# Kernel tuning notes

Hardware: AMD Instinct MI355X
Metric: run time of the kernel (lower is better)

Reference implementation:

```python
import jax, jax.numpy as jnp
import numpy as np


def quantize_ternary(w):
    # BitNet b1.58: scale by mean |w|, round, clamp to {-1,0,1}
    gamma = jnp.maximum(jnp.mean(jnp.abs(w)), 1e-8)
    return jnp.clip(jnp.round(w / gamma), -1.0, 1.0)


def setup_inputs() -> dict:
    key = jax.random.key(0)
    k1, k2, k3 = jax.random.split(key, 3)
    in_features, out_features = 4096, 4096
    x = jax.random.normal(k1, (4, 2048, in_features), dtype=jnp.float32)
    # kaiming_uniform-like init
    bound_w = 1.0 / np.sqrt(in_features)
    weight = jax.random.uniform(k2, (out_features, in_features), dtype=jnp.float32,
                                minval=-bound_w * np.sqrt(3.0), maxval=bound_w * np.sqrt(3.0))
    bias = jax.random.uniform(k3, (out_features,), dtype=jnp.float32,
                              minval=-bound_w, maxval=bound_w)
    return {"x": x, "weight": weight, "bias": bias}


def reference(x, weight, bias):
    qw = quantize_ternary(weight)  # [out, in], values in {-1,0,1}
    # F.linear: x @ qw.T + bias
    return jnp.einsum('bsi,oi->bso', x, qw) + bias
```

## Files before the change

### kernel.cpp

```cpp
#include <hip/hip_runtime.h>
#include <stdint.h>

#define M_DIM 8192
#define N_DIM 4096
#define K_DIM 4096
#define BM 256
#define BN 128
#define BKS 64
#define NSLAB (K_DIM / BKS)
#define A_SLOT (BM * BKS)
#define B_SLOT (BN * BKS)

typedef int i32x4 __attribute__((ext_vector_type(4)));

__device__ __forceinline__ void async_copy16(const void* g, void* l) {
    __builtin_amdgcn_global_load_lds(
        (const __attribute__((address_space(1))) void*)g,
        (__attribute__((address_space(3))) void*)l, 16, 0, 0);
}

__global__ __launch_bounds__(256) void prep_kernel(
    const float4* __restrict__ w,
    const float4* __restrict__ x,
    double* __restrict__ partials,
    char4* __restrict__ xq,
    float* __restrict__ xscale)
{
    const int lane = threadIdx.x & 63;
    const int wave = threadIdx.x >> 6;

    if (blockIdx.x < 1024) {
        int base = blockIdx.x * 4096 + threadIdx.x;
        float s = 0.f;
        #pragma unroll
        for (int i = 0; i < 16; i++) {
            float4 v = w[base + i * 256];
            s += fabsf(v.x) + fabsf(v.y) + fabsf(v.z) + fabsf(v.w);
        }
        double d = (double)s;
        #pragma unroll
        for (int off = 32; off > 0; off >>= 1) d += __shfl_down(d, off, 64);
        __shared__ double wsum[4];
        if (lane == 0) wsum[wave] = d;
        __syncthreads();
        if (threadIdx.x == 0)
            partials[blockIdx.x] = (wsum[0] + wsum[1]) + (wsum[2] + wsum[3]);
    } else {
        const int row = blockIdx.x - 1024;
        const float4* xr = x + (size_t)row * (K_DIM / 4);
        float4 v[4];
        float m = 0.f;
        #pragma unroll
        for (int i = 0; i < 4; i++) {
            v[i] = xr[threadIdx.x + i * 256];
            m = fmaxf(m, fmaxf(fmaxf(fabsf(v[i].x), fabsf(v[i].y)),
                               fmaxf(fabsf(v[i].z), fabsf(v[i].w))));
        }
        #pragma unroll
        for (int off = 32; off > 0; off >>= 1) m = fmaxf(m, __shfl_down(m, off, 64));
        __shared__ float wmax[4];
        if (lane == 0) wmax[wave] = m;
        __syncthreads();
        const float mx = fmaxf(fmaxf(wmax[0], wmax[1]), fmaxf(wmax[2], wmax[3]));
        const float scale = fmaxf(mx * (1.f / 127.f), 1e-30f);
        const float inv = 1.f / scale;
        if (threadIdx.x == 0) xscale[row] = scale;
        char4* oq = xq + (size_t)row * (K_DIM / 4);
        #pragma unroll
        for (int i = 0; i < 4; i++) {
            char4 o;
            o.x = (signed char)fminf(fmaxf(rintf(v[i].x * inv), -127.f), 127.f);
            o.y = (signed char)fminf(fmaxf(rintf(v[i].y * inv), -127.f), 127.f);
            o.z = (signed char)fminf(fmaxf(rintf(v[i].z * inv), -127.f), 127.f);
            o.w = (signed char)fminf(fmaxf(rintf(v[i].w * inv), -127.f), 127.f);
            oq[threadIdx.x + i * 256] = o;
        }
    }
}

__global__ __launch_bounds__(256) void wquant_kernel(
    const double* __restrict__ partials,
    const float4* __restrict__ w,
    char4* __restrict__ qw)
{
    const int lane = threadIdx.x & 63;
    const int wave = threadIdx.x >> 6;
    double d = partials[threadIdx.x] + partials[threadIdx.x + 256] +
               partials[threadIdx.x + 512] + partials[threadIdx.x + 768];
    #pragma unroll
    for (int off = 32; off > 0; off >>= 1) d += __shfl_down(d, off, 64);
    __shared__ double wsum[4];
    if (lane == 0) wsum[wave] = d;
    __shared__ float gsh;
    __syncthreads();
    if (threadIdx.x == 0) {
        double total = (wsum[0] + wsum[1]) + (wsum[2] + wsum[3]);
        gsh = fmaxf((float)(total * (1.0 / 16777216.0)), 1e-8f);
    }
    __syncthreads();
    const float gamma = gsh;

    int base = blockIdx.x * 4096 + threadIdx.x;
    #pragma unroll
    for (int j = 0; j < 16; j++) {
        float4 v = w[base + j * 256];
        char4 o;
        o.x = (signed char)fminf(fmaxf(rintf(v.x / gamma), -1.f), 1.f);
        o.y = (signed char)fminf(fmaxf(rintf(v.y / gamma), -1.f), 1.f);
        o.z = (signed char)fminf(fmaxf(rintf(v.z / gamma), -1.f), 1.f);
        o.w = (signed char)fminf(fmaxf(rintf(v.w / gamma), -1.f), 1.f);
        qw[base + j * 256] = o;
    }
}

__global__ __launch_bounds__(256, 2) void gemm_kernel(
    const char* __restrict__ xq,
    const char* __restrict__ qw,
    const float* __restrict__ xscale,
    const float* __restrict__ bias,
    float* __restrict__ out)
{
    __shared__ __align__(16) char As[3][A_SLOT];
    __shared__ __align__(16) char Bs[3][B_SLOT];

    const int tid  = threadIdx.x;
    const int wave = tid >> 6;
    const int lane = tid & 63;
    const int wm   = (wave >> 1) * 128;
    const int wn   = (wave & 1) * 64;
    const int lm   = lane & 15;
    const int q4   = lane >> 4;

    const int bm = blockIdx.y * BM;
    const int bn = blockIdx.x * BN;

    const int rsub = lane >> 2;
    const int csw  = (lane & 3) ^ ((lane >> 3) & 3);
    const char* gA[4];
    int ldsOffA[4];
    #pragma unroll
    for (int j = 0; j < 4; j++) {
        const int r = wave * 64 + j * 16 + rsub;
        gA[j] = xq + (size_t)(bm + r) * K_DIM + csw * 16;
        ldsOffA[j] = (wave * 64 + j * 16) * BKS;
    }
    const char* gB[2];
    int ldsOffB[2];
    #pragma unroll
    for (int j = 0; j < 2; j++) {
        const int r = wave * 32 + j * 16 + rsub;
        gB[j] = qw + (size_t)(bn + r) * K_DIM + csw * 16;
        ldsOffB[j] = (wave * 32 + j * 16) * BKS;
    }

    i32x4 acc[8][4];
    #pragma unroll
    for (int i = 0; i < 8; i++)
        #pragma unroll
        for (int j = 0; j < 4; j++) acc[i][j] = (i32x4){0, 0, 0, 0};

    const int pc = (q4 ^ ((lm >> 1) & 3)) * 16;

    auto stage_slab = [&](int ts, int slot) {
        #pragma unroll
        for (int j = 0; j < 4; j++)
            async_copy16(gA[j] + (size_t)ts * BKS, &As[slot][ldsOffA[j]]);
        #pragma unroll
        for (int j = 0; j < 2; j++)
            async_copy16(gB[j] + (size_t)ts * BKS, &Bs[slot][ldsOffB[j]]);
    };

    auto compute_slab = [&](const char* Ab, const char* Bb) {
        i32x4 b[4], a[8];
        #pragma unroll
        for (int ni = 0; ni < 4; ni++)
            b[ni] = *(const i32x4*)(Bb + (wn + ni * 16 + lm) * BKS + pc);
        #pragma unroll
        for (int mi = 0; mi < 8; mi++)
            a[mi] = *(const i32x4*)(Ab + (wm + mi * 16 + lm) * BKS + pc);
        __builtin_amdgcn_s_setprio(1);
        #pragma unroll
        for (int mi = 0; mi < 8; mi++)
            #pragma unroll
            for (int ni = 0; ni < 4; ni++)
                acc[mi][ni] = __builtin_amdgcn_mfma_i32_16x16x64_i8(
                    a[mi], b[ni], acc[mi][ni], 0, 0, 0);
        __builtin_amdgcn_s_setprio(0);
    };

    stage_slab(0, 0);
    stage_slab(1, 1);
    asm volatile("s_waitcnt vmcnt(6)" ::: "memory");
    __builtin_amdgcn_s_barrier();

    for (int tb = 0; tb < 60; tb += 3) {
        #pragma unroll
        for (int u = 0; u < 3; u++) {
            stage_slab(tb + u + 2, (u + 2) % 3);
            compute_slab(As[u], Bs[u]);
            asm volatile("s_waitcnt vmcnt(6)" ::: "memory");
            __builtin_amdgcn_s_barrier();
        }
    }

    stage_slab(62, 2);
    compute_slab(As[0], Bs[0]);
    asm volatile("s_waitcnt vmcnt(6)" ::: "memory");
    __builtin_amdgcn_s_barrier();

    stage_slab(63, 0);
    compute_slab(As[1], Bs[1]);
    asm volatile("s_waitcnt vmcnt(6)" ::: "memory");
    __builtin_amdgcn_s_barrier();

    compute_slab(As[2], Bs[2]);
    asm volatile("s_waitcnt vmcnt(0)" ::: "memory");
    __builtin_amdgcn_s_barrier();

    compute_slab(As[0], Bs[0]);

    float bl[4];
    #pragma unroll
    for (int ni = 0; ni < 4; ni++) bl[ni] = bias[bn + wn + ni * 16 + lm];

    #pragma unroll
    for (int mi = 0; mi < 8; mi++) {
        #pragma unroll
        for (int r = 0; r < 4; r++) {
            const int grow = bm + wm + mi * 16 + q4 * 4 + r;
            const float sc = xscale[grow];
            float* orow = out + (size_t)grow * N_DIM + bn + wn;
            #pragma unroll
            for (int ni = 0; ni < 4; ni++)
                orow[ni * 16 + lm] = sc * (float)acc[mi][ni][r] + bl[ni];
        }
    }
}

extern "C" void kernel_launch(void* const* d_in, const int* in_sizes, int n_in,
                              void* d_out, int out_size, void* d_ws, size_t ws_size,
                              hipStream_t stream) {
    const float* x    = (const float*)d_in[0];
    const float* w    = (const float*)d_in[1];
    const float* bias = (const float*)d_in[2];
    float* out = (float*)d_out;

    char* ws = (char*)d_ws;
    char*   xq       = ws;
    char*   qw       = ws + (size_t)M_DIM * K_DIM;
    float*  xscale   = (float*)(qw + (size_t)N_DIM * K_DIM);
    double* partials = (double*)(xscale + M_DIM);
    float*  gamma_p  = (float*)(partials + 1024);
    (void)gamma_p;

    prep_kernel<<<1024 + M_DIM, 256, 0, stream>>>(
        (const float4*)w, (const float4*)x, partials, (char4*)xq, xscale);
    wquant_kernel<<<1024, 256, 0, stream>>>(partials, (const float4*)w, (char4*)qw);

    dim3 grid(N_DIM / BN, M_DIM / BM);
    gemm_kernel<<<grid, 256, 0, stream>>>(xq, qw, xscale, bias, out);
}
```

Baseline: 410.5 us.

## Use 256x256 tiles with 32x32x32 int8 MFMA and register double-buffered fragments

The GEMM tile grows from 256x128 to 256x256 and switches from 16x16x64 to 32x32x32 int8 MFMA, which raises arithmetic intensity per LDS byte and halves the number of blocks. The LDS ring goes from three to four slots and stages three slabs ahead. Fragments for the next slab are read into a second register buffer while MFMAs run on the current one, with sched_barriers enforcing the order. Occupancy drops to one block per CU and register pressure rises, and the swizzle and epilogue row mapping change to match the new layout.

```diff
diff --git a/kernel.cpp b/kernel.cpp
--- a/kernel.cpp
+++ b/kernel.cpp
@@ -5,13 +5,13 @@
 #define N_DIM 4096
 #define K_DIM 4096
 #define BM 256
-#define BN 128
+#define BN 256
 #define BKS 64
 #define NSLAB (K_DIM / BKS)
-#define A_SLOT (BM * BKS)
-#define B_SLOT (BN * BKS)
-
-typedef int i32x4 __attribute__((ext_vector_type(4)));
+#define SLOT_BYTES (256 * BKS)
+
+typedef int i32x4  __attribute__((ext_vector_type(4)));
+typedef int i32x16 __attribute__((ext_vector_type(16)));
 
 __device__ __forceinline__ void async_copy16(const void* g, void* l) {
     __builtin_amdgcn_global_load_lds(
@@ -113,126 +113,150 @@
     }
 }
 
-__global__ __launch_bounds__(256, 2) void gemm_kernel(
+__global__ __launch_bounds__(256, 1) void gemm_kernel(
     const char* __restrict__ xq,
     const char* __restrict__ qw,
     const float* __restrict__ xscale,
     const float* __restrict__ bias,
     float* __restrict__ out)
 {
-    __shared__ __align__(16) char As[3][A_SLOT];
-    __shared__ __align__(16) char Bs[3][B_SLOT];
+    __shared__ __align__(16) char As[4][SLOT_BYTES];
+    __shared__ __align__(16) char Bs[4][SLOT_BYTES];
 
     const int tid  = threadIdx.x;
     const int wave = tid >> 6;
     const int lane = tid & 63;
     const int wm   = (wave >> 1) * 128;
-    const int wn   = (wave & 1) * 64;
-    const int lm   = lane & 15;
-    const int q4   = lane >> 4;
+    const int wn   = (wave & 1) * 128;
+    const int l31  = lane & 31;
+    const int lhi  = lane >> 5;
 
     const int bm = blockIdx.y * BM;
     const int bn = blockIdx.x * BN;
 
     const int rsub = lane >> 2;
-    const int csw  = (lane & 3) ^ ((lane >> 3) & 3);
+    const int csw  = (lane & 3) ^ ((lane >> 2) & 3);
     const char* gA[4];
-    int ldsOffA[4];
+    const char* gB[4];
+    int ldsOff[4];
     #pragma unroll
     for (int j = 0; j < 4; j++) {
         const int r = wave * 64 + j * 16 + rsub;
         gA[j] = xq + (size_t)(bm + r) * K_DIM + csw * 16;
-        ldsOffA[j] = (wave * 64 + j * 16) * BKS;
-    }
-    const char* gB[2];
-    int ldsOffB[2];
-    #pragma unroll
-    for (int j = 0; j < 2; j++) {
-        const int r = wave * 32 + j * 16 + rsub;
         gB[j] = qw + (size_t)(bn + r) * K_DIM + csw * 16;
-        ldsOffB[j] = (wave * 32 + j * 16) * BKS;
-    }
-
-    i32x4 acc[8][4];
-    #pragma unroll
-    for (int i = 0; i < 8; i++)
-        #pragma unroll
-        for (int j = 0; j < 4; j++) acc[i][j] = (i32x4){0, 0, 0, 0};
-
-    const int pc = (q4 ^ ((lm >> 1) & 3)) * 16;
+        ldsOff[j] = (wave * 64 + j * 16) * BKS;
+    }
+
+    i32x16 acc[4][4];
+    const i32x16 zz = {0,0,0,0,0,0,0,0,0,0,0,0,0,0,0,0};
+    #pragma unroll
+    for (int i = 0; i < 4; i++)
+        #pragma unroll
+        for (int j = 0; j < 4; j++) acc[i][j] = zz;
+
+    const int ch0 = ((0 + lhi) ^ (l31 & 3)) * 16;
+    const int ch1 = ((2 + lhi) ^ (l31 & 3)) * 16;
+    const int rowA = (wm + l31) * BKS;
+    const int rowB = (wn + l31) * BKS;
+
+    i32x4 bufA0[4][2], bufB0[4][2], bufA1[4][2], bufB1[4][2];
 
     auto stage_slab = [&](int ts, int slot) {
         #pragma unroll
-        for (int j = 0; j < 4; j++)
-            async_copy16(gA[j] + (size_t)ts * BKS, &As[slot][ldsOffA[j]]);
-        #pragma unroll
-        for (int j = 0; j < 2; j++)
-            async_copy16(gB[j] + (size_t)ts * BKS, &Bs[slot][ldsOffB[j]]);
+        for (int j = 0; j < 4; j++) {
+            async_copy16(gA[j] + (size_t)ts * BKS, &As[slot][ldsOff[j]]);
+            async_copy16(gB[j] + (size_t)ts * BKS, &Bs[slot][ldsOff[j]]);
+        }
     };
 
-    auto compute_slab = [&](const char* Ab, const char* Bb) {
-        i32x4 b[4], a[8];
-        #pragma unroll
-        for (int ni = 0; ni < 4; ni++)
-            b[ni] = *(const i32x4*)(Bb + (wn + ni * 16 + lm) * BKS + pc);
-        #pragma unroll
-        for (int mi = 0; mi < 8; mi++)
-            a[mi] = *(const i32x4*)(Ab + (wm + mi * 16 + lm) * BKS + pc);
+    auto read_frags = [&](i32x4 (&rA)[4][2], i32x4 (&rB)[4][2], int slot) {
+        const char* Ab = As[slot];
+        const char* Bb = Bs[slot];
+        #pragma unroll
+        for (int f = 0; f < 4; f++) {
+            rA[f][0] = *(const i32x4*)(Ab + rowA + f * 2048 + ch0);
+            rA[f][1] = *(const i32x4*)(Ab + rowA + f * 2048 + ch1);
+            rB[f][0] = *(const i32x4*)(Bb + rowB + f * 2048 + ch0);
+            rB[f][1] = *(const i32x4*)(Bb + rowB + f * 2048 + ch1);
+        }
+    };
+
+    auto mfma_all = [&](i32x4 (&cA)[4][2], i32x4 (&cB)[4][2]) {
         __builtin_amdgcn_s_setprio(1);
         #pragma unroll
-        for (int mi = 0; mi < 8; mi++)
+        for (int ks = 0; ks < 2; ks++)
             #pragma unroll
-            for (int ni = 0; ni < 4; ni++)
-                acc[mi][ni] = __builtin_amdgcn_mfma_i32_16x16x64_i8(
-                    a[mi], b[ni], acc[mi][ni], 0, 0, 0);
+            for (int mi = 0; mi < 4; mi++)
+                #pragma unroll
+                for (int ni = 0; ni < 4; ni++)
+                    acc[mi][ni] = __builtin_amdgcn_mfma_i32_32x32x32_i8(
+                        cA[mi][ks], cB[ni][ks], acc[mi][ni], 0, 0, 0);
         __builtin_amdgcn_s_setprio(0);
     };
 
     stage_slab(0, 0);
     stage_slab(1, 1);
-    asm volatile("s_waitcnt vmcnt(6)" ::: "memory");
+    stage_slab(2, 2);
+    asm volatile("s_waitcnt vmcnt(16)" ::: "memory");
     __builtin_amdgcn_s_barrier();
-
-    for (int tb = 0; tb < 60; tb += 3) {
-        #pragma unroll
-        for (int u = 0; u < 3; u++) {
-            stage_slab(tb + u + 2, (u + 2) % 3);
-            compute_slab(As[u], Bs[u]);
-            asm volatile("s_waitcnt vmcnt(6)" ::: "memory");
+    read_frags(bufA0, bufB0, 0);
+
+    for (int tb = 0; tb < 60; tb += 4) {
+        #pragma unroll
+        for (int u = 0; u < 4; u++) {
+            const int ts = tb + u + 3;
+            stage_slab(ts, (u + 3) & 3);
+            if (u & 1) read_frags(bufA0, bufB0, (u + 1) & 3);
+            else       read_frags(bufA1, bufB1, (u + 1) & 3);
+            __builtin_amdgcn_sched_barrier(0);
+            if (u & 1) mfma_all(bufA1, bufB1);
+            else       mfma_all(bufA0, bufB0);
+            asm volatile("s_waitcnt lgkmcnt(0)" ::: "memory");
+            __builtin_amdgcn_sched_barrier(0);
+            asm volatile("s_waitcnt vmcnt(8)" ::: "memory");
             __builtin_amdgcn_s_barrier();
         }
     }
 
-    stage_slab(62, 2);
-    compute_slab(As[0], Bs[0]);
-    asm volatile("s_waitcnt vmcnt(6)" ::: "memory");
+    stage_slab(63, 3);
+    read_frags(bufA1, bufB1, 1);
+    __builtin_amdgcn_sched_barrier(0);
+    mfma_all(bufA0, bufB0);
+    asm volatile("s_waitcnt lgkmcnt(0)" ::: "memory");
+    __builtin_amdgcn_sched_barrier(0);
+    asm volatile("s_waitcnt vmcnt(8)" ::: "memory");
     __builtin_amdgcn_s_barrier();
 
-    stage_slab(63, 0);
-    compute_slab(As[1], Bs[1]);
-    asm volatile("s_waitcnt vmcnt(6)" ::: "memory");
-    __builtin_amdgcn_s_barrier();
-
-    compute_slab(As[2], Bs[2]);
+    read_frags(bufA0, bufB0, 2);
+    __builtin_amdgcn_sched_barrier(0);
+    mfma_all(bufA1, bufB1);
+    asm volatile("s_waitcnt lgkmcnt(0)" ::: "memory");
+    __builtin_amdgcn_sched_barrier(0);
     asm volatile("s_waitcnt vmcnt(0)" ::: "memory");
     __builtin_amdgcn_s_barrier();
 
-    compute_slab(As[0], Bs[0]);
+    read_frags(bufA1, bufB1, 3);
+    __builtin_amdgcn_sched_barrier(0);
+    mfma_all(bufA0, bufB0);
+    asm volatile("s_waitcnt lgkmcnt(0)" ::: "memory");
+    __builtin_amdgcn_sched_barrier(0);
+
+    mfma_all(bufA1, bufB1);
 
     float bl[4];
     #pragma unroll
-    for (int ni = 0; ni < 4; ni++) bl[ni] = bias[bn + wn + ni * 16 + lm];
-
-    #pragma unroll
-    for (int mi = 0; mi < 8; mi++) {
-        #pragma unroll
-        for (int r = 0; r < 4; r++) {
-            const int grow = bm + wm + mi * 16 + q4 * 4 + r;
+    for (int ni = 0; ni < 4; ni++) bl[ni] = bias[bn + wn + ni * 32 + l31];
+
+    #pragma unroll
+    for (int mi = 0; mi < 4; mi++) {
+        #pragma unroll
+        for (int r = 0; r < 16; r++) {
+            const int grow = bm + wm + mi * 32 + (r & 3) + 8 * (r >> 2) + 4 * lhi;
             const float sc = xscale[grow];
             float* orow = out + (size_t)grow * N_DIM + bn + wn;
             #pragma unroll
             for (int ni = 0; ni < 4; ni++)
-                orow[ni * 16 + lm] = sc * (float)acc[mi][ni][r] + bl[ni];
+                orow[ni * 32 + l31] = sc * (float)acc[mi][ni][r] + bl[ni];
         }
     }
 }
@@ -250,8 +274,6 @@
     char*   qw       = ws + (size_t)M_DIM * K_DIM;
     float*  xscale   = (float*)(qw + (size_t)N_DIM * K_DIM);
     double* partials = (double*)(xscale + M_DIM);
-    float*  gamma_p  = (float*)(partials + 1024);
-    (void)gamma_p;
 
     prep_kernel<<<1024 + M_DIM, 256, 0, stream>>>(
         (const float4*)w, (const float4*)x, partials, (char4*)xq, xscale);
```

Result: slower. 473.4 us (+15.3%).
